# Kernel tuning notes

Measured on AMD Instinct MI355X. Metric: run time of the kernel, lower is better.

## Reference

```python
import jax, jax.numpy as jnp
import numpy as np

B, L, IDIM = 2, 4096, 2048
N_HEADS, N_GROUPS, HEAD_DIM = 16, 4, 128
GROUP_SIZE = N_HEADS // N_GROUPS
WINDOW = 1024
SCALE = 256.0 ** -0.5  # query_pre_attn_scalar = 256
EPS = 1e-6


def setup_inputs() -> dict:
    key = jax.random.key(0)
    ks = jax.random.split(key, 8)
    x = jax.random.normal(ks[0], (B, L, IDIM), dtype=jnp.float32)
    # realistic RoPE tables
    inv_freq = 1.0 / (10000.0 ** (np.arange(0, HEAD_DIM, 2, dtype=np.float32) / HEAD_DIM))
    t = np.arange(L, dtype=np.float32)
    freqs = np.outer(t, inv_freq)                      # [L, HEAD_DIM//2]
    emb = np.concatenate([freqs, freqs], axis=-1)      # [L, HEAD_DIM]
    cos = jnp.asarray(np.cos(emb), dtype=jnp.float32)
    sin = jnp.asarray(np.sin(emb), dtype=jnp.float32)
    s = 0.02
    Wq = jax.random.normal(ks[1], (IDIM, N_HEADS * HEAD_DIM), dtype=jnp.float32) * s
    Wk = jax.random.normal(ks[2], (IDIM, N_GROUPS * HEAD_DIM), dtype=jnp.float32) * s
    Wv = jax.random.normal(ks[3], (IDIM, N_GROUPS * HEAD_DIM), dtype=jnp.float32) * s
    Wo = jax.random.normal(ks[4], (N_HEADS * HEAD_DIM, IDIM), dtype=jnp.float32) * s
    qn_w = jnp.ones((HEAD_DIM,), dtype=jnp.float32)
    kn_w = jnp.ones((HEAD_DIM,), dtype=jnp.float32)
    return {"x": x, "cos": cos, "sin": sin, "Wq": Wq, "Wk": Wk, "Wv": Wv, "Wo": Wo, "qn_w": qn_w, "kn_w": kn_w}


def _rmsnorm(x, w):
    var = jnp.mean(jnp.square(x), axis=-1, keepdims=True)
    return x * jax.lax.rsqrt(var + EPS) * w


def _rope(x, cos, sin):
    # x: [b, h, l, d]; cos/sin: [l, d]
    d2 = x.shape[-1] // 2
    x1, x2 = x[..., :d2], x[..., d2:]
    rot = jnp.concatenate([-x2, x1], axis=-1)
    return x * cos[None, None] + rot * sin[None, None]


def reference(x, cos, sin, Wq, Wk, Wv, Wo, qn_w, kn_w):
    b, l, _ = x.shape
    q = (x @ Wq).reshape(b, l, N_HEADS, HEAD_DIM).transpose(0, 2, 1, 3)   # b h l d
    k = (x @ Wk).reshape(b, l, N_GROUPS, HEAD_DIM).transpose(0, 2, 1, 3)  # b g l d
    v = (x @ Wv).reshape(b, l, N_GROUPS, HEAD_DIM).transpose(0, 2, 1, 3)  # b g l d
    q = _rmsnorm(q, qn_w)
    k = _rmsnorm(k, kn_w)
    q = _rope(q, cos, sin)
    k = _rope(k, cos, sin)
    k = jnp.repeat(k, GROUP_SIZE, axis=1)  # b h l d
    v = jnp.repeat(v, GROUP_SIZE, axis=1)
    dots = jnp.einsum('bhid,bhjd->bhij', q, k) * SCALE
    i = jnp.arange(l)[:, None]
    j = jnp.arange(l)[None, :]
    allowed = (j <= i) & (j > i - WINDOW)  # causal sliding window
    dots = jnp.where(allowed[None, None], dots, -jnp.inf)
    attn = jax.nn.softmax(dots, axis=-1)
    out = jnp.einsum('bhij,bhjd->bhid', attn, v)
    out = out.transpose(0, 2, 1, 3).reshape(b, l, N_HEADS * HEAD_DIM)
    return out @ Wo
```

## Files before the change

### kernel.cpp

```cpp
#include <hip/hip_runtime.h>
#include <hip/hip_bf16.h>

typedef __hip_bfloat16 bf16;
typedef __attribute__((ext_vector_type(8))) __bf16 bf16x8;
typedef __attribute__((ext_vector_type(4))) float f32x4;

#define MFMA16(a, b, c) __builtin_amdgcn_mfma_f32_16x16x32_bf16((a), (b), (c), 0, 0, 0)

static __device__ __forceinline__ void gload_lds16(const void* g, void* l) {
    typedef const __attribute__((address_space(1))) unsigned gq_t;
    typedef __attribute__((address_space(3))) unsigned ls_t;
    __builtin_amdgcn_global_load_lds((gq_t*)g, (ls_t*)l, 16, 0, 0);
}

static __device__ __forceinline__ unsigned short f2bfbits(float f) {
    bf16 h = __float2bfloat16(f);
    return *reinterpret_cast<unsigned short*>(&h);
}

__global__ __launch_bounds__(256) void cvt_bf16_kernel(const float* __restrict__ in,
                                                       bf16* __restrict__ out, int n) {
    int i = (blockIdx.x * 256 + threadIdx.x) * 8;
    if (i < n) {
        float4 a = *reinterpret_cast<const float4*>(in + i);
        float4 b = *reinterpret_cast<const float4*>(in + i + 4);
        bf16 tmp[8];
        tmp[0] = __float2bfloat16(a.x); tmp[1] = __float2bfloat16(a.y);
        tmp[2] = __float2bfloat16(a.z); tmp[3] = __float2bfloat16(a.w);
        tmp[4] = __float2bfloat16(b.x); tmp[5] = __float2bfloat16(b.y);
        tmp[6] = __float2bfloat16(b.z); tmp[7] = __float2bfloat16(b.w);
        *reinterpret_cast<uint4*>(out + i) = *reinterpret_cast<const uint4*>(tmp);
    }
}

__global__ __launch_bounds__(256) void transpose_wqkv_kernel(const float* __restrict__ Wq,
                                                             const float* __restrict__ Wk,
                                                             const float* __restrict__ Wv,
                                                             bf16* __restrict__ out) {
    __shared__ float tile[32][33];
    int k0 = blockIdx.x * 32;
    int n0 = blockIdx.y * 32;
    int tx = threadIdx.x & 31, ty = threadIdx.x >> 5;
#pragma unroll
    for (int i = 0; i < 4; ++i) {
        int k = k0 + ty + i * 8, n = n0 + tx;
        float v;
        if (n < 2048)      v = Wq[(size_t)k * 2048 + n];
        else if (n < 2560) v = Wk[(size_t)k * 512 + (n - 2048)];
        else               v = Wv[(size_t)k * 512 + (n - 2560)];
        tile[ty + i * 8][tx] = v;
    }
    __syncthreads();
#pragma unroll
    for (int i = 0; i < 4; ++i)
        out[(size_t)(n0 + ty + i * 8) * 2048 + k0 + tx] = __float2bfloat16(tile[tx][ty + i * 8]);
}

__global__ __launch_bounds__(256) void transpose_w_kernel(const float* __restrict__ in,
                                                          bf16* __restrict__ out) {
    __shared__ float tile[32][33];
    int k0 = blockIdx.x * 32, n0 = blockIdx.y * 32;
    int tx = threadIdx.x & 31, ty = threadIdx.x >> 5;
#pragma unroll
    for (int i = 0; i < 4; ++i)
        tile[ty + i * 8][tx] = in[(size_t)(k0 + ty + i * 8) * 2048 + n0 + tx];
    __syncthreads();
#pragma unroll
    for (int i = 0; i < 4; ++i)
        out[(size_t)(n0 + ty + i * 8) * 2048 + k0 + tx] = __float2bfloat16(tile[tx][ty + i * 8]);
}

template <int NFRAG, bool OUT_F32>
__global__ __launch_bounds__(512, 2) void gemm8p_kernel(const bf16* __restrict__ A,
                                                        const bf16* __restrict__ BT,
                                                        void* __restrict__ Cv,
                                                        int M, int N, int K, int nbn) {
    constexpr int BN = NFRAG * 64;
    constexpr int PB = NFRAG;
    __shared__ bf16 As[2][256 * 64];
    __shared__ bf16 Bs[2][BN * 64];
    int t = threadIdx.x;
    int lane = t & 63, w = t >> 6;
    int wm = w >> 2, wn = w & 3;
    int lr = lane & 15, lq = lane >> 4;
    int lin = blockIdx.x;
    int cpx = gridDim.x >> 3;
    int wg = (lin & 7) * cpx + (lin >> 3);
    int bm = wg / nbn, bn = wg % nbn;
    const bf16* Ab = A + (size_t)bm * 256 * K;
    const bf16* Bb = BT + (size_t)bn * BN * K;

    auto stA = [&](int slot, int kt, int piece) {
        int idx = piece * 512 + t;
        int r = idx >> 3, c8 = idx & 7;
        gload_lds16(Ab + (size_t)r * K + kt * 64 + ((c8 ^ (r & 7)) * 8), &As[slot][idx * 8]);
    };
    auto stB = [&](int slot, int kt, int piece) {
        int idx = piece * 512 + t;
        int r = idx >> 3, c8 = idx & 7;
        gload_lds16(Bb + (size_t)r * K + kt * 64 + ((c8 ^ (r & 7)) * 8), &Bs[slot][idx * 8]);
    };

    f32x4 acc[8][NFRAG] = {};
    bf16x8 bq[NFRAG][2], af[2][2];

    auto readB = [&](int slot) {
#pragma unroll
        for (int n = 0; n < NFRAG; ++n)
#pragma unroll
            for (int ks = 0; ks < 2; ++ks) {
                int ro = wn * (NFRAG * 16) + n * 16 + lr;
                int ch = (ks * 4 + lq) ^ (ro & 7);
                bq[n][ks] = *reinterpret_cast<const bf16x8*>(&Bs[slot][ro * 64 + ch * 8]);
            }
    };
    auto readA = [&](int mbase, int slot) {
#pragma unroll
        for (int mi = 0; mi < 2; ++mi)
#pragma unroll
            for (int ks = 0; ks < 2; ++ks) {
                int ro = wm * 128 + (mbase + mi) * 16 + lr;
                int ch = (ks * 4 + lq) ^ (ro & 7);
                af[mi][ks] = *reinterpret_cast<const bf16x8*>(&As[slot][ro * 64 + ch * 8]);
            }
    };
    auto mf = [&](int mbase) {
#pragma unroll
        for (int mi = 0; mi < 2; ++mi)
#pragma unroll
            for (int n = 0; n < NFRAG; ++n)
#pragma unroll
                for (int ks = 0; ks < 2; ++ks)
                    acc[mbase + mi][n] = MFMA16(af[mi][ks], bq[n][ks], acc[mbase + mi][n]);
    };

#define GATE_PB()                                                          \
    do {                                                                   \
        if constexpr (NFRAG == 4) asm volatile("s_waitcnt vmcnt(4)" ::: "memory"); \
        else                      asm volatile("s_waitcnt vmcnt(3)" ::: "memory"); \
    } while (0)
#define PHASE_TAIL()                                                       \
    do {                                                                   \
        __builtin_amdgcn_s_barrier();                                      \
        asm volatile("s_waitcnt lgkmcnt(0)" ::: "memory");                 \
    } while (0)
#define MFMA_CLUSTER(mb)                                                   \
    do {                                                                   \
        __builtin_amdgcn_s_setprio(1);                                     \
        mf(mb);                                                            \
        __builtin_amdgcn_s_setprio(0);                                     \
        __builtin_amdgcn_s_barrier();                                      \
    } while (0)

    int nkt = K >> 6;
#pragma unroll
    for (int p = 0; p < 4; ++p) stA(0, 0, p);
#pragma unroll
    for (int p = 0; p < PB; ++p) stB(0, 0, p);
#pragma unroll
    for (int p = 0; p < PB; ++p) stB(1, 1, p);
    GATE_PB();
    __builtin_amdgcn_s_barrier();

    int nI = nkt >> 1;
    for (int I = 0; I < nI; ++I) {
        int T = I << 1;
        bool s2 = (T + 2) < nkt, s3 = (T + 3) < nkt;
        readB(0); readA(0, 0);
#pragma unroll
        for (int p = 0; p < 4; ++p) stA(1, T + 1, p);
        PHASE_TAIL();
        MFMA_CLUSTER(0);
        readA(2, 0);
        if (s2) { stB(0, T + 2, 0); stB(0, T + 2, 1); }
        PHASE_TAIL();
        MFMA_CLUSTER(2);
        readA(4, 0);
        if (s2) {
#pragma unroll
            for (int p = 2; p < PB; ++p) stB(0, T + 2, p);
        }
        PHASE_TAIL();
        MFMA_CLUSTER(4);
        readA(6, 0);
        if (s2) GATE_PB();
        else    asm volatile("s_waitcnt vmcnt(0)" ::: "memory");
        PHASE_TAIL();
        MFMA_CLUSTER(6);
        readB(1); readA(0, 1);
        if (s2) {
#pragma unroll
            for (int p = 0; p < 4; ++p) stA(0, T + 2, p);
        }
        PHASE_TAIL();
        MFMA_CLUSTER(0);
        readA(2, 1);
        if (s3) { stB(1, T + 3, 0); stB(1, T + 3, 1); }
        PHASE_TAIL();
        MFMA_CLUSTER(2);
        readA(4, 1);
        if (s3) {
#pragma unroll
            for (int p = 2; p < PB; ++p) stB(1, T + 3, p);
        }
        PHASE_TAIL();
        MFMA_CLUSTER(4);
        readA(6, 1);
        if (s3) GATE_PB();
        else    asm volatile("s_waitcnt vmcnt(0)" ::: "memory");
        PHASE_TAIL();
        MFMA_CLUSTER(6);
    }
#undef GATE_PB
#undef PHASE_TAIL
#undef MFMA_CLUSTER

#pragma unroll
    for (int m = 0; m < 8; ++m)
#pragma unroll
        for (int n = 0; n < NFRAG; ++n) {
            int row = bm * 256 + wm * 128 + m * 16 + lq * 4;
            int col = bn * BN + wn * (NFRAG * 16) + n * 16 + lr;
#pragma unroll
            for (int j = 0; j < 4; ++j) {
                if (OUT_F32)
                    ((float*)Cv)[(size_t)(row + j) * N + col] = acc[m][n][j];
                else
                    ((bf16*)Cv)[(size_t)(row + j) * N + col] = __float2bfloat16(acc[m][n][j]);
            }
        }
}

__global__ __launch_bounds__(256) void normrope_kernel(const bf16* __restrict__ qkv,
                                                       const float* __restrict__ cosT,
                                                       const float* __restrict__ sinT,
                                                       const float* __restrict__ qnw,
                                                       const float* __restrict__ knw,
                                                       bf16* __restrict__ qh,
                                                       bf16* __restrict__ kh,
                                                       bf16* __restrict__ vt) {
    int t = threadIdx.x;
    int lane = t & 63, wv = t >> 6;
    int blk = blockIdx.x;
    int r = blk / 6;
    int s = (blk % 6) * 4 + wv;
    int b = r >> 12, l = r & 4095;
    int e0 = lane * 2;
    const bf16* src = qkv + (size_t)r * 3072 + s * 128;
    ushort2 xu = *reinterpret_cast<const ushort2*>(src + e0);
    float v0 = __uint_as_float((unsigned)xu.x << 16);
    float v1 = __uint_as_float((unsigned)xu.y << 16);
    if (s < 20) {
        float ss = v0 * v0 + v1 * v1;
#pragma unroll
        for (int d = 1; d < 64; d <<= 1) ss += __shfl_xor(ss, d, 64);
        float rn = rsqrtf(ss * (1.0f / 128.0f) + 1e-6f);
        const float* wn = (s < 16) ? qnw : knw;
        float2 wv2 = *reinterpret_cast<const float2*>(wn + e0);
        float xn0 = v0 * rn * wv2.x;
        float xn1 = v1 * rn * wv2.y;
        float xp0 = __shfl_xor(xn0, 32, 64);
        float xp1 = __shfl_xor(xn1, 32, 64);
        float r0 = (lane < 32) ? -xp0 : xp0;
        float r1 = (lane < 32) ? -xp1 : xp1;
        float2 c2 = *reinterpret_cast<const float2*>(cosT + (size_t)l * 128 + e0);
        float2 s2 = *reinterpret_cast<const float2*>(sinT + (size_t)l * 128 + e0);
        float o0 = xn0 * c2.x + r0 * s2.x;
        float o1 = xn1 * c2.y + r1 * s2.y;
        ushort2 ou;
        if (s < 16) {
            const float scl = 0.0625f * 1.44269504088896f;
            ou.x = f2bfbits(o0 * scl);
            ou.y = f2bfbits(o1 * scl);
            bf16* dst = qh + ((size_t)(b * 16 + s) * 4096 + l) * 128;
            *reinterpret_cast<ushort2*>(dst + e0) = ou;
        } else {
            int g = s - 16;
            ou.x = f2bfbits(o0);
            ou.y = f2bfbits(o1);
            int sw = (l & 7) << 3;
            bf16* dst = kh + ((size_t)(b * 4 + g) * 4096 + l) * 128;
            *reinterpret_cast<ushort2*>(dst + (e0 ^ sw)) = ou;
        }
    } else {
        int g = s - 20;
        bf16* dst = vt + (size_t)(b * 4 + g) * 128 * 4096;
        int base = l & ~63, cj = l & 63;
        int pos = (cj & 0x23) | ((cj & 16) >> 2) | ((cj & 12) << 1);
        int d0 = e0, d1 = e0 + 1;
        dst[(size_t)d0 * 4096 + base + (pos ^ ((d0 & 7) << 3))] = __float2bfloat16(v0);
        dst[(size_t)d1 * 4096 + base + (pos ^ ((d1 & 7) << 3))] = __float2bfloat16(v1);
    }
}

__global__ __launch_bounds__(512, 4) void attn_kernel(const bf16* __restrict__ qh,
                                                      const bf16* __restrict__ kh,
                                                      const bf16* __restrict__ vt,
                                                      bf16* __restrict__ ao) {
    __shared__ bf16 Ks[2][64 * 128];
    __shared__ bf16 Vs[2][128 * 64];
    int t = threadIdx.x;
    int lane = t & 63, w = t >> 6;
    int lr = lane & 15, lq = lane >> 4;
    int qs = blockIdx.x * 128;
    int bh = blockIdx.y;
    int b = bh >> 4, h = bh & 15, g = h >> 2;
    const bf16* qp = qh + ((size_t)(b * 16 + h) * 4096 + qs + w * 16) * 128;
    const bf16* kp = kh + (size_t)(b * 4 + g) * 4096 * 128;
    const bf16* vp = vt + (size_t)(b * 4 + g) * 128 * 4096;

    bf16x8 aq[4];
#pragma unroll
    for (int kk = 0; kk < 4; ++kk)
        aq[kk] = *reinterpret_cast<const bf16x8*>(qp + (size_t)lr * 128 + kk * 32 + lq * 8);

    f32x4 o[8] = {};
    float lsum = 0.f;
    int row0 = qs + w * 16;
    int qi = row0 + lr;
    int t0w = max(0, row0 - 1023) >> 6;
    int t1w = row0 >> 6;
    int t0 = max(0, qs - 1023) >> 6;
    int t1 = (qs + 112) >> 6;

    auto stage = [&](int buf, int kt) {
        int j0 = kt * 64;
        const bf16* kg = kp + (size_t)j0 * 128;
#pragma unroll
        for (int i = 0; i < 2; ++i) {
            int c = i * 512 + t;
            gload_lds16(kg + c * 8, &Ks[buf][c * 8]);
        }
#pragma unroll
        for (int i = 0; i < 2; ++i) {
            int c = i * 512 + t;
            int d = c >> 3, co = (c & 7) * 8;
            gload_lds16(vp + (size_t)d * 4096 + j0 + co, &Vs[buf][c * 8]);
        }
    };

    stage(0, t0);
    __syncthreads();
    int cur = 0;

    for (int kt = t0; kt <= t1; ++kt) {
        int j0 = kt * 64;
        if (kt < t1) stage(cur ^ 1, kt + 1);
        if (kt >= t0w && kt <= t1w) {
            f32x4 s[4] = {};
            __builtin_amdgcn_s_setprio(1);
#pragma unroll
            for (int jt = 0; jt < 4; ++jt) {
                int r = jt * 16 + lr;
                int rs = (r & 7) << 3;
#pragma unroll
                for (int kk = 0; kk < 4; ++kk) {
                    int c = kk * 32 + lq * 8;
                    bf16x8 bk = *reinterpret_cast<const bf16x8*>(&Ks[cur][r * 128 + (c ^ rs)]);
                    s[jt] = MFMA16(bk, aq[kk], s[jt]);
                }
            }
            __builtin_amdgcn_s_setprio(0);
            if (kt <= t0w + 1 || kt == t1w) {
#pragma unroll
                for (int jt = 0; jt < 4; ++jt)
#pragma unroll
                    for (int j = 0; j < 4; ++j) {
                        int kj = j0 + jt * 16 + lq * 4 + j;
                        if (!(kj <= qi && kj > qi - 1024)) s[jt][j] = -1e30f;
                    }
            }
            unsigned pk[4][2];
#pragma unroll
            for (int jt = 0; jt < 4; ++jt)
#pragma unroll
                for (int hh = 0; hh < 2; ++hh) {
                    float p0 = exp2f(s[jt][2 * hh] - 11.5415603f);
                    float p1 = exp2f(s[jt][2 * hh + 1] - 11.5415603f);
                    lsum += p0 + p1;
                    asm("v_cvt_pk_bf16_f32 %0, %1, %2" : "=v"(pk[jt][hh]) : "v"(p0), "v"(p1));
                }
            __builtin_amdgcn_s_setprio(1);
#pragma unroll
            for (int kk2 = 0; kk2 < 2; ++kk2) {
                union { unsigned u[4]; bf16x8 v; } pu;
                pu.u[0] = pk[2 * kk2][0];
                pu.u[1] = pk[2 * kk2][1];
                pu.u[2] = pk[2 * kk2 + 1][0];
                pu.u[3] = pk[2 * kk2 + 1][1];
#pragma unroll
                for (int dt = 0; dt < 8; ++dt) {
                    int r = dt * 16 + lr;
                    int c = kk2 * 32 + lq * 8;
                    bf16x8 bv = *reinterpret_cast<const bf16x8*>(&Vs[cur][r * 64 + (c ^ ((r & 7) << 3))]);
                    o[dt] = MFMA16(pu.v, bv, o[dt]);
                }
            }
            __builtin_amdgcn_s_setprio(0);
        }
        __syncthreads();
        cur ^= 1;
    }
    float lt = lsum;
    lt += __shfl_xor(lt, 16, 64);
    lt += __shfl_xor(lt, 32, 64);
    float linv = 1.0f / lt;
    float lv[4];
#pragma unroll
    for (int j = 0; j < 4; ++j)
        lv[j] = __shfl(linv, lq * 4 + j, 64);
#pragma unroll
    for (int dt = 0; dt < 8; ++dt)
#pragma unroll
        for (int j = 0; j < 4; ++j) {
            float val = o[dt][j] * lv[j];
            ao[((size_t)(b * 4096 + row0 + lq * 4 + j)) * 2048 + h * 128 + dt * 16 + lr] =
                __float2bfloat16(val);
        }
}

extern "C" void kernel_launch(void* const* d_in, const int* in_sizes, int n_in,
                              void* d_out, int out_size, void* d_ws, size_t ws_size,
                              hipStream_t stream) {
    const float* x    = (const float*)d_in[0];
    const float* cosT = (const float*)d_in[1];
    const float* sinT = (const float*)d_in[2];
    const float* Wq   = (const float*)d_in[3];
    const float* Wk   = (const float*)d_in[4];
    const float* Wv   = (const float*)d_in[5];
    const float* Wo   = (const float*)d_in[6];
    const float* qnw  = (const float*)d_in[7];
    const float* knw  = (const float*)d_in[8];

    char* ws = (char*)d_ws;
    bf16* xb    = (bf16*)(ws);
    bf16* wqkvT = (bf16*)(ws + 33554432);
    bf16* woT   = (bf16*)(ws + 46137344);
    bf16* qh    = (bf16*)(ws + 54525952);
    bf16* kh    = (bf16*)(ws + 88080384);
    bf16* vt    = (bf16*)(ws + 96468992);
    bf16* ao    = xb;
    bf16* qkv   = (bf16*)d_out;

    cvt_bf16_kernel<<<8192, 256, 0, stream>>>(x, xb, 16777216);
    transpose_wqkv_kernel<<<dim3(64, 96), 256, 0, stream>>>(Wq, Wk, Wv, wqkvT);
    transpose_w_kernel<<<dim3(64, 64), 256, 0, stream>>>(Wo, woT);
    gemm8p_kernel<3, false><<<512, 512, 0, stream>>>(xb, wqkvT, (void*)qkv, 8192, 3072, 2048, 16);
    normrope_kernel<<<49152, 256, 0, stream>>>(qkv, cosT, sinT, qnw, knw, qh, kh, vt);
    attn_kernel<<<dim3(32, 32), 512, 0, stream>>>(qh, kh, vt, ao);
    gemm8p_kernel<4, true><<<256, 512, 0, stream>>>(ao, woT, d_out, 8192, 2048, 2048, 8);
}
```

Before: 357.0 us.

## Split V transpose into tiled kernel and double attention query rows per wave

Several changes land together. The V transpose moves out of normrope into a new LDS-tiled vtrans kernel, so the scattered 2-byte global stores from normrope go away. The attention kernel now gives each wave 32 query rows instead of 16, so every staged K/V tile feeds twice the MFMA work, and it remaps blocks to a 1D grid that groups heads. The pipeline now uses explicit vmcnt waits with raw s_barrier, and the QKV GEMM template and tile parameters change. In exchange the attention kernel needs more registers and has lower occupancy (launch bounds 512,2), and the grid has fewer blocks.

```diff
diff --git a/kernel.cpp b/kernel.cpp
--- a/kernel.cpp
+++ b/kernel.cpp
@@ -237,63 +237,79 @@
                                                        const float* __restrict__ qnw,
                                                        const float* __restrict__ knw,
                                                        bf16* __restrict__ qh,
-                                                       bf16* __restrict__ kh,
-                                                       bf16* __restrict__ vt) {
+                                                       bf16* __restrict__ kh) {
     int t = threadIdx.x;
     int lane = t & 63, wv = t >> 6;
     int blk = blockIdx.x;
-    int r = blk / 6;
-    int s = (blk % 6) * 4 + wv;
+    int r = blk / 5;
+    int s = (blk % 5) * 4 + wv;
     int b = r >> 12, l = r & 4095;
     int e0 = lane * 2;
     const bf16* src = qkv + (size_t)r * 3072 + s * 128;
     ushort2 xu = *reinterpret_cast<const ushort2*>(src + e0);
     float v0 = __uint_as_float((unsigned)xu.x << 16);
     float v1 = __uint_as_float((unsigned)xu.y << 16);
-    if (s < 20) {
-        float ss = v0 * v0 + v1 * v1;
-#pragma unroll
-        for (int d = 1; d < 64; d <<= 1) ss += __shfl_xor(ss, d, 64);
-        float rn = rsqrtf(ss * (1.0f / 128.0f) + 1e-6f);
-        const float* wn = (s < 16) ? qnw : knw;
-        float2 wv2 = *reinterpret_cast<const float2*>(wn + e0);
-        float xn0 = v0 * rn * wv2.x;
-        float xn1 = v1 * rn * wv2.y;
-        float xp0 = __shfl_xor(xn0, 32, 64);
-        float xp1 = __shfl_xor(xn1, 32, 64);
-        float r0 = (lane < 32) ? -xp0 : xp0;
-        float r1 = (lane < 32) ? -xp1 : xp1;
-        float2 c2 = *reinterpret_cast<const float2*>(cosT + (size_t)l * 128 + e0);
-        float2 s2 = *reinterpret_cast<const float2*>(sinT + (size_t)l * 128 + e0);
-        float o0 = xn0 * c2.x + r0 * s2.x;
-        float o1 = xn1 * c2.y + r1 * s2.y;
-        ushort2 ou;
-        if (s < 16) {
-            const float scl = 0.0625f * 1.44269504088896f;
-            ou.x = f2bfbits(o0 * scl);
-            ou.y = f2bfbits(o1 * scl);
-            bf16* dst = qh + ((size_t)(b * 16 + s) * 4096 + l) * 128;
-            *reinterpret_cast<ushort2*>(dst + e0) = ou;
-        } else {
-            int g = s - 16;
-            ou.x = f2bfbits(o0);
-            ou.y = f2bfbits(o1);
-            int sw = (l & 7) << 3;
-            bf16* dst = kh + ((size_t)(b * 4 + g) * 4096 + l) * 128;
-            *reinterpret_cast<ushort2*>(dst + (e0 ^ sw)) = ou;
-        }
+    float ss = v0 * v0 + v1 * v1;
+#pragma unroll
+    for (int d = 1; d < 64; d <<= 1) ss += __shfl_xor(ss, d, 64);
+    float rn = rsqrtf(ss * (1.0f / 128.0f) + 1e-6f);
+    const float* wn = (s < 16) ? qnw : knw;
+    float2 wv2 = *reinterpret_cast<const float2*>(wn + e0);
+    float xn0 = v0 * rn * wv2.x;
+    float xn1 = v1 * rn * wv2.y;
+    float xp0 = __shfl_xor(xn0, 32, 64);
+    float xp1 = __shfl_xor(xn1, 32, 64);
+    float r0 = (lane < 32) ? -xp0 : xp0;
+    float r1 = (lane < 32) ? -xp1 : xp1;
+    float2 c2 = *reinterpret_cast<const float2*>(cosT + (size_t)l * 128 + e0);
+    float2 s2 = *reinterpret_cast<const float2*>(sinT + (size_t)l * 128 + e0);
+    float o0 = xn0 * c2.x + r0 * s2.x;
+    float o1 = xn1 * c2.y + r1 * s2.y;
+    ushort2 ou;
+    if (s < 16) {
+        const float scl = 0.0625f * 1.44269504088896f;
+        ou.x = f2bfbits(o0 * scl);
+        ou.y = f2bfbits(o1 * scl);
+        bf16* dst = qh + ((size_t)(b * 16 + s) * 4096 + l) * 128;
+        *reinterpret_cast<ushort2*>(dst + e0) = ou;
     } else {
-        int g = s - 20;
-        bf16* dst = vt + (size_t)(b * 4 + g) * 128 * 4096;
-        int base = l & ~63, cj = l & 63;
-        int pos = (cj & 0x23) | ((cj & 16) >> 2) | ((cj & 12) << 1);
-        int d0 = e0, d1 = e0 + 1;
-        dst[(size_t)d0 * 4096 + base + (pos ^ ((d0 & 7) << 3))] = __float2bfloat16(v0);
-        dst[(size_t)d1 * 4096 + base + (pos ^ ((d1 & 7) << 3))] = __float2bfloat16(v1);
-    }
-}
-
-__global__ __launch_bounds__(512, 4) void attn_kernel(const bf16* __restrict__ qh,
+        int g = s - 16;
+        ou.x = f2bfbits(o0);
+        ou.y = f2bfbits(o1);
+        int sw = (l & 7) << 3;
+        bf16* dst = kh + ((size_t)(b * 4 + g) * 4096 + l) * 128;
+        *reinterpret_cast<ushort2*>(dst + (e0 ^ sw)) = ou;
+    }
+}
+
+__global__ __launch_bounds__(256) void vtrans_kernel(const bf16* __restrict__ qkv,
+                                                     bf16* __restrict__ vt) {
+    __shared__ bf16 tile[64][132];
+    int t = threadIdx.x;
+    int l0 = blockIdx.x * 64;
+    int bg = blockIdx.y;
+    int b = bg >> 2, g = bg & 3;
+    const bf16* src = qkv + ((size_t)(b * 4096 + l0)) * 3072 + 2560 + g * 128;
+#pragma unroll
+    for (int i = 0; i < 4; ++i) {
+        int c = i * 256 + t;
+        int r = c >> 4, c16 = c & 15;
+        uint4 v = *reinterpret_cast<const uint4*>(src + (size_t)r * 3072 + c16 * 8);
+        *reinterpret_cast<uint2*>(&tile[r][c16 * 8]) = make_uint2(v.x, v.y);
+        *reinterpret_cast<uint2*>(&tile[r][c16 * 8 + 4]) = make_uint2(v.z, v.w);
+    }
+    __syncthreads();
+    bf16* dst = vt + (size_t)bg * 128 * 4096 + l0;
+    int cj = t & 63;
+    int pos = (cj & 0x23) | ((cj & 16) >> 2) | ((cj & 12) << 1);
+#pragma unroll
+    for (int dd = 0; dd < 32; ++dd) {
+        int d = (t >> 6) * 32 + dd;
+        dst[(size_t)d * 4096 + (pos ^ ((d & 7) << 3))] = tile[cj][d];
+    }
+}
+
+__global__ __launch_bounds__(512, 2) void attn_kernel(const bf16* __restrict__ qh,
                                                       const bf16* __restrict__ kh,
                                                       const bf16* __restrict__ vt,
                                                       bf16* __restrict__ ao) {
@@ -302,26 +318,31 @@
     int t = threadIdx.x;
     int lane = t & 63, w = t >> 6;
     int lr = lane & 15, lq = lane >> 4;
-    int qs = blockIdx.x * 128;
-    int bh = blockIdx.y;
+    int bid = blockIdx.x;
+    int bh = (bid & 7) * 4 + (bid >> 7);
+    int qs = ((bid >> 3) & 15) * 256;
     int b = bh >> 4, h = bh & 15, g = h >> 2;
-    const bf16* qp = qh + ((size_t)(b * 16 + h) * 4096 + qs + w * 16) * 128;
+    int row0 = qs + w * 32;
+    const bf16* qp = qh + ((size_t)(b * 16 + h) * 4096 + row0) * 128;
     const bf16* kp = kh + (size_t)(b * 4 + g) * 4096 * 128;
     const bf16* vp = vt + (size_t)(b * 4 + g) * 128 * 4096;
 
-    bf16x8 aq[4];
-#pragma unroll
-    for (int kk = 0; kk < 4; ++kk)
-        aq[kk] = *reinterpret_cast<const bf16x8*>(qp + (size_t)lr * 128 + kk * 32 + lq * 8);
-
-    f32x4 o[8] = {};
-    float lsum = 0.f;
-    int row0 = qs + w * 16;
-    int qi = row0 + lr;
-    int t0w = max(0, row0 - 1023) >> 6;
+    bf16x8 aq[2][4];
+#pragma unroll
+    for (int g2 = 0; g2 < 2; ++g2)
+#pragma unroll
+        for (int kk = 0; kk < 4; ++kk)
+            aq[g2][kk] = *reinterpret_cast<const bf16x8*>(qp + (size_t)(g2 * 16 + lr) * 128 + kk * 32 + lq * 8);
+
+    f32x4 o0[8] = {}, o1[8] = {};
+    float lsum0 = 0.f, lsum1 = 0.f;
+    int qi0 = row0 + lr, qi1 = row0 + 16 + lr;
+    int sA = max(0, row0 - 1023) >> 6;
+    int sB = max(0, row0 + 16 - 1023) >> 6;
     int t1w = row0 >> 6;
+    int t0w = sA;
     int t0 = max(0, qs - 1023) >> 6;
-    int t1 = (qs + 112) >> 6;
+    int t1 = (qs + 255) >> 6;
 
     auto stage = [&](int buf, int kt) {
         int j0 = kt * 64;
@@ -340,14 +361,19 @@
     };
 
     stage(0, t0);
-    __syncthreads();
     int cur = 0;
 
     for (int kt = t0; kt <= t1; ++kt) {
-        int j0 = kt * 64;
-        if (kt < t1) stage(cur ^ 1, kt + 1);
+        if (kt < t1) {
+            stage(cur ^ 1, kt + 1);
+            asm volatile("s_waitcnt vmcnt(4)" ::: "memory");
+        } else {
+            asm volatile("s_waitcnt vmcnt(0)" ::: "memory");
+        }
+        __builtin_amdgcn_s_barrier();
         if (kt >= t0w && kt <= t1w) {
-            f32x4 s[4] = {};
+            int j0 = kt * 64;
+            f32x4 s0[4] = {}, s1[4] = {};
             __builtin_amdgcn_s_setprio(1);
 #pragma unroll
             for (int jt = 0; jt < 4; ++jt) {
@@ -357,65 +383,87 @@
                 for (int kk = 0; kk < 4; ++kk) {
                     int c = kk * 32 + lq * 8;
                     bf16x8 bk = *reinterpret_cast<const bf16x8*>(&Ks[cur][r * 128 + (c ^ rs)]);
-                    s[jt] = MFMA16(bk, aq[kk], s[jt]);
+                    s0[jt] = MFMA16(bk, aq[0][kk], s0[jt]);
+                    s1[jt] = MFMA16(bk, aq[1][kk], s1[jt]);
                 }
             }
             __builtin_amdgcn_s_setprio(0);
-            if (kt <= t0w + 1 || kt == t1w) {
+            if (kt <= sA + 1 || kt == t1w) {
 #pragma unroll
                 for (int jt = 0; jt < 4; ++jt)
 #pragma unroll
                     for (int j = 0; j < 4; ++j) {
                         int kj = j0 + jt * 16 + lq * 4 + j;
-                        if (!(kj <= qi && kj > qi - 1024)) s[jt][j] = -1e30f;
+                        if (!(kj <= qi0 && kj > qi0 - 1024)) s0[jt][j] = -1e30f;
                     }
             }
-            unsigned pk[4][2];
+            if (kt <= sB + 1 || kt == t1w) {
+#pragma unroll
+                for (int jt = 0; jt < 4; ++jt)
+#pragma unroll
+                    for (int j = 0; j < 4; ++j) {
+                        int kj = j0 + jt * 16 + lq * 4 + j;
+                        if (!(kj <= qi1 && kj > qi1 - 1024)) s1[jt][j] = -1e30f;
+                    }
+            }
+            unsigned pk0[4][2], pk1[4][2];
 #pragma unroll
             for (int jt = 0; jt < 4; ++jt)
 #pragma unroll
                 for (int hh = 0; hh < 2; ++hh) {
-                    float p0 = exp2f(s[jt][2 * hh] - 11.5415603f);
-                    float p1 = exp2f(s[jt][2 * hh + 1] - 11.5415603f);
-                    lsum += p0 + p1;
-                    asm("v_cvt_pk_bf16_f32 %0, %1, %2" : "=v"(pk[jt][hh]) : "v"(p0), "v"(p1));
+                    float p0 = exp2f(s0[jt][2 * hh] - 11.5415603f);
+                    float p1 = exp2f(s0[jt][2 * hh + 1] - 11.5415603f);
+                    lsum0 += p0 + p1;
+                    asm("v_cvt_pk_bf16_f32 %0, %1, %2" : "=v"(pk0[jt][hh]) : "v"(p0), "v"(p1));
+                }
+#pragma unroll
+            for (int jt = 0; jt < 4; ++jt)
+#pragma unroll
+                for (int hh = 0; hh < 2; ++hh) {
+                    float p0 = exp2f(s1[jt][2 * hh] - 11.5415603f);
+                    float p1 = exp2f(s1[jt][2 * hh + 1] - 11.5415603f);
+                    lsum1 += p0 + p1;
+                    asm("v_cvt_pk_bf16_f32 %0, %1, %2" : "=v"(pk1[jt][hh]) : "v"(p0), "v"(p1));
                 }
             __builtin_amdgcn_s_setprio(1);
 #pragma unroll
             for (int kk2 = 0; kk2 < 2; ++kk2) {
-                union { unsigned u[4]; bf16x8 v; } pu;
-                pu.u[0] = pk[2 * kk2][0];
-                pu.u[1] = pk[2 * kk2][1];
-                pu.u[2] = pk[2 * kk2 + 1][0];
-                pu.u[3] = pk[2 * kk2 + 1][1];
+                union { unsigned u[4]; bf16x8 v; } pu0, pu1;
+                pu0.u[0] = pk0[2 * kk2][0]; pu0.u[1] = pk0[2 * kk2][1];
+                pu0.u[2] = pk0[2 * kk2 + 1][0]; pu0.u[3] = pk0[2 * kk2 + 1][1];
+                pu1.u[0] = pk1[2 * kk2][0]; pu1.u[1] = pk1[2 * kk2][1];
+                pu1.u[2] = pk1[2 * kk2 + 1][0]; pu1.u[3] = pk1[2 * kk2 + 1][1];
 #pragma unroll
                 for (int dt = 0; dt < 8; ++dt) {
                     int r = dt * 16 + lr;
                     int c = kk2 * 32 + lq * 8;
                     bf16x8 bv = *reinterpret_cast<const bf16x8*>(&Vs[cur][r * 64 + (c ^ ((r & 7) << 3))]);
-                    o[dt] = MFMA16(pu.v, bv, o[dt]);
+                    o0[dt] = MFMA16(pu0.v, bv, o0[dt]);
+                    o1[dt] = MFMA16(pu1.v, bv, o1[dt]);
                 }
             }
             __builtin_amdgcn_s_setprio(0);
         }
-        __syncthreads();
+        __builtin_amdgcn_s_barrier();
         cur ^= 1;
     }
-    float lt = lsum;
-    lt += __shfl_xor(lt, 16, 64);
-    lt += __shfl_xor(lt, 32, 64);
-    float linv = 1.0f / lt;
-    float lv[4];
-#pragma unroll
-    for (int j = 0; j < 4; ++j)
-        lv[j] = __shfl(linv, lq * 4 + j, 64);
+    float lt0 = lsum0, lt1 = lsum1;
+    lt0 += __shfl_xor(lt0, 16, 64);  lt0 += __shfl_xor(lt0, 32, 64);
+    lt1 += __shfl_xor(lt1, 16, 64);  lt1 += __shfl_xor(lt1, 32, 64);
+    float li0 = 1.0f / lt0, li1 = 1.0f / lt1;
+    float lv0[4], lv1[4];
+#pragma unroll
+    for (int j = 0; j < 4; ++j) {
+        lv0[j] = __shfl(li0, lq * 4 + j, 64);
+        lv1[j] = __shfl(li1, lq * 4 + j, 64);
+    }
 #pragma unroll
     for (int dt = 0; dt < 8; ++dt)
 #pragma unroll
         for (int j = 0; j < 4; ++j) {
-            float val = o[dt][j] * lv[j];
-            ao[((size_t)(b * 4096 + row0 + lq * 4 + j)) * 2048 + h * 128 + dt * 16 + lr] =
-                __float2bfloat16(val);
+            size_t base = (size_t)(b * 4096 + row0 + lq * 4 + j) * 2048 + h * 128 + dt * 16 + lr;
+            ao[base] = __float2bfloat16(o0[dt][j] * lv0[j]);
+            ao[base + (size_t)16 * 2048] = __float2bfloat16(o1[dt][j] * lv1[j]);
         }
 }
 
@@ -445,8 +493,9 @@
     cvt_bf16_kernel<<<8192, 256, 0, stream>>>(x, xb, 16777216);
     transpose_wqkv_kernel<<<dim3(64, 96), 256, 0, stream>>>(Wq, Wk, Wv, wqkvT);
     transpose_w_kernel<<<dim3(64, 64), 256, 0, stream>>>(Wo, woT);
-    gemm8p_kernel<3, false><<<512, 512, 0, stream>>>(xb, wqkvT, (void*)qkv, 8192, 3072, 2048, 16);
-    normrope_kernel<<<49152, 256, 0, stream>>>(qkv, cosT, sinT, qnw, knw, qh, kh, vt);
-    attn_kernel<<<dim3(32, 32), 512, 0, stream>>>(qh, kh, vt, ao);
+    gemm8p_kernel<4, false><<<384, 512, 0, stream>>>(xb, wqkvT, (void*)qkv, 8192, 3072, 2048, 12);
+    normrope_kernel<<<40960, 256, 0, stream>>>(qkv, cosT, sinT, qnw, knw, qh, kh);
+    vtrans_kernel<<<dim3(64, 8), 256, 0, stream>>>(qkv, vt);
+    attn_kernel<<<512, 512, 0, stream>>>(qh, kh, vt, ao);
     gemm8p_kernel<4, true><<<256, 512, 0, stream>>>(ao, woT, d_out, 8192, 2048, 2048, 8);
 }
```

New measurement: 366.6 us. 2.7% more time.
